# Kernel optimization log

Measured on AMD Instinct MI355X. Metric: run time of the kernel, lower is better.

Reference implementation:

```python
import jax, jax.numpy as jnp
import numpy as np

B, LQ, LK, D, H = 8, 1024, 1024, 1024, 8
DH = D // H  # per-head dim (att_units // num_heads, and V head dim since V = k)
LN_EPS = 1e-5


def setup_inputs() -> dict:
    key = jax.random.key(0)
    ks = jax.random.split(key, 8)
    s = 1.0 / np.sqrt(D)
    return {
        "q": jax.random.normal(ks[0], (B, LQ, D), dtype=jnp.float32),
        "k": jax.random.normal(ks[1], (B, LK, D), dtype=jnp.float32),
        "Wq": jax.random.normal(ks[2], (D, D), dtype=jnp.float32) * s,
        "bq": jnp.zeros((D,), dtype=jnp.float32),
        "Wk": jax.random.normal(ks[3], (D, D), dtype=jnp.float32) * s,
        "bk": jnp.zeros((D,), dtype=jnp.float32),
        "ln_gamma": jnp.ones((D,), dtype=jnp.float32),
        "ln_beta": jnp.zeros((D,), dtype=jnp.float32),
    }


def _layer_norm(x, gamma, beta):
    mu = jnp.mean(x, axis=-1, keepdims=True)
    var = jnp.mean(jnp.square(x - mu), axis=-1, keepdims=True)
    return (x - mu) * jax.lax.rsqrt(var + LN_EPS) * gamma + beta


def reference(q, k, Wq, bq, Wk, bk, ln_gamma, ln_beta):
    # q: [B, LQ, D], k: [B, LK, D]
    Q = q @ Wq + bq                      # [B, LQ, D]
    K = k @ Wk + bk                      # [B, LK, D]
    V = k                                # V is the raw key input (no projection)
    Qh = Q.reshape(B, LQ, H, DH)         # split(att_units//H, -1)+concat(0) == head reshape
    Kh = K.reshape(B, LK, H, DH)
    Vh = V.reshape(B, LK, H, DH)
    sim = jnp.einsum("bqhd,bkhd->bhqk", Qh, Kh) / np.sqrt(DH).astype(np.float32)
    attn = jax.nn.softmax(sim, axis=-1)  # [B, H, LQ, LK]
    att_h = jnp.einsum("bhqk,bkhd->bqhd", attn, Vh).reshape(B, LQ, D)
    att_h = att_h * 0.1 + q * 0.9        # residual blend
    att_h = _layer_norm(att_h, ln_gamma, ln_beta)
    return att_h  # ff_units_list == [] -> ff is None -> ff_h = att_h
```

## Files before the change

kernel.cpp:

```cpp
#include <hip/hip_runtime.h>
#include <hip/hip_bf16.h>
#include <cstdint>

#define BATCH 8
#define SEQ   1024
#define DMODEL 1024
#define NHEAD 8
#define DHEAD 128

using short8 = __attribute__((ext_vector_type(8))) short;
using f32x4  = __attribute__((ext_vector_type(4))) float;
typedef unsigned short u16;

__device__ inline u16 f2bf(float f) {
    union { float f; uint32_t u; } v; v.f = f;
    uint32_t r = (v.u + 0x7FFFu + ((v.u >> 16) & 1u)) >> 16;
    return (u16)r;
}

__device__ inline float exp2_fast(float x) { return __builtin_amdgcn_exp2f(x); }

__device__ inline uint32_t cvtpk_bf16(float a, float b) {
    uint32_t r;
    asm("v_cvt_pk_bf16_f32 %0, %1, %2" : "=v"(r) : "v"(a), "v"(b));
    return r;
}

#define GLL16(g, l)                                                                        \
    __builtin_amdgcn_global_load_lds((__attribute__((address_space(1))) const uint32_t*)(g), \
                                     (__attribute__((address_space(3))) uint32_t*)(l), 16, 0, 0)

__global__ __launch_bounds__(256) void conv_bf16(const float* __restrict__ q,
                                                 u16* __restrict__ dst) {
    size_t e = ((size_t)blockIdx.x * 256 + threadIdx.x) * 8;
    float4 a = *(const float4*)(q + e);
    float4 b = *(const float4*)(q + e + 4);
    uint4 r;
    r.x = (uint32_t)f2bf(a.x) | ((uint32_t)f2bf(a.y) << 16);
    r.y = (uint32_t)f2bf(a.z) | ((uint32_t)f2bf(a.w) << 16);
    r.z = (uint32_t)f2bf(b.x) | ((uint32_t)f2bf(b.y) << 16);
    r.w = (uint32_t)f2bf(b.z) | ((uint32_t)f2bf(b.w) << 16);
    *(uint4*)(dst + e) = r;
}

__global__ void transpose_conv(const float* __restrict__ Wq,
                               const float* __restrict__ Wk,
                               const float* __restrict__ kin,
                               u16* __restrict__ WqT,
                               u16* __restrict__ WkT,
                               u16* __restrict__ Vt,
                               u16* __restrict__ kb) {
    __shared__ float tile[32][33];
    int z = blockIdx.z;
    const float* src;
    u16* dst;
    u16* sdst = nullptr;
    if (z == 0)      { src = Wq; dst = WqT; }
    else if (z == 1) { src = Wk; dst = WkT; }
    else {
        src  = kin + (size_t)(z - 2) * DMODEL * SEQ;
        dst  = Vt  + (size_t)(z - 2) * DMODEL * SEQ;
        sdst = kb  + (size_t)(z - 2) * DMODEL * SEQ;
    }
    int x  = blockIdx.x * 32 + threadIdx.x;
    int y0 = blockIdx.y * 32;
    for (int i = threadIdx.y; i < 32; i += 8) {
        float v = src[(size_t)(y0 + i) * 1024 + x];
        tile[i][threadIdx.x] = v;
        if (sdst) sdst[(size_t)(y0 + i) * 1024 + x] = f2bf(v);
    }
    __syncthreads();
    int xo  = y0 + threadIdx.x;
    int yo0 = blockIdx.x * 32;
    for (int i = threadIdx.y; i < 32; i += 8)
        dst[(size_t)(yo0 + i) * 1024 + xo] = f2bf(tile[threadIdx.x][i]);
}

__global__ __launch_bounds__(256, 4) void gemm_dual(const u16* __restrict__ Aq,
                                                    const u16* __restrict__ Ak,
                                                    const u16* __restrict__ BTq,
                                                    const u16* __restrict__ BTk,
                                                    const float* __restrict__ biasq,
                                                    const float* __restrict__ biask,
                                                    u16* __restrict__ Outq,
                                                    u16* __restrict__ Outk) {
    __shared__ __align__(16) u16 As[2][128 * 32];
    __shared__ __align__(16) u16 Bs[2][128 * 32];

    int bid = blockIdx.x;
    int half = bid >> 9;
    int b2 = bid & 511;
    const u16* A  = half ? Ak  : Aq;
    const u16* BT = half ? BTk : BTq;
    const float* bias = half ? biask : biasq;
    u16* Out = half ? Outk : Outq;
    float scale = half ? 1.0f : (0.08838834764831845f * 1.4426950408889634f);

    int swz = (b2 & 7) * 64 + (b2 >> 3);
    int mt = swz >> 3, nt = swz & 7;
    int m0 = mt * 128, n0 = nt * 128;

    int t = threadIdx.x, lane = t & 63, w = t >> 6;
    int wm = w >> 1, wn = w & 1;
    int lr = lane & 15, lg = lane >> 4;

    const u16* pa[2];
    const u16* pb[2];
#pragma unroll
    for (int i = 0; i < 2; ++i) {
        int L = (w * 2 + i) * 64 + lane;
        int rp = L >> 3, ss = L & 7;
        int u = ss ^ (rp & 7);
        int row = (rp << 1) | (u >> 2);
        int g = u & 3;
        pa[i] = A  + (size_t)(m0 + row) * 1024 + g * 8;
        pb[i] = BT + (size_t)(n0 + row) * 1024 + g * 8;
    }
    int aoff[4], boff[4];
#pragma unroll
    for (int f = 0; f < 4; ++f) {
        int rowA = wm * 64 + f * 16 + lr;
        int sA = (((rowA & 1) << 2) | lg) ^ ((rowA >> 1) & 7);
        aoff[f] = (rowA >> 1) * 64 + sA * 8;
        int rowB = wn * 64 + f * 16 + lr;
        int sB = (((rowB & 1) << 2) | lg) ^ ((rowB >> 1) & 7);
        boff[f] = (rowB >> 1) * 64 + sB * 8;
    }

    f32x4 acc[4][4] = {};

#define GSTAGE(buf)                                         \
    {                                                       \
        _Pragma("unroll")                                   \
        for (int i = 0; i < 2; ++i) {                       \
            GLL16(pa[i], &As[buf][(w * 2 + i) * 512]);      \
            GLL16(pb[i], &Bs[buf][(w * 2 + i) * 512]);      \
            pa[i] += 32;                                    \
            pb[i] += 32;                                    \
        }                                                   \
    }

    GSTAGE(0);
    __syncthreads();

    int cur = 0;
    for (int k0 = 0; k0 < DMODEL; k0 += 32) {
        if (k0 + 32 < DMODEL) GSTAGE(cur ^ 1);
        short8 af[4], bfr[4];
#pragma unroll
        for (int f = 0; f < 4; ++f) {
            af[f]  = *(const short8*)&As[cur][aoff[f]];
            bfr[f] = *(const short8*)&Bs[cur][boff[f]];
        }
        __builtin_amdgcn_s_setprio(1);
#pragma unroll
        for (int fm = 0; fm < 4; ++fm)
#pragma unroll
            for (int fn = 0; fn < 4; ++fn)
                acc[fm][fn] = __builtin_amdgcn_mfma_f32_16x16x32_bf16(af[fm], bfr[fn], acc[fm][fn], 0, 0, 0);
        __builtin_amdgcn_s_setprio(0);
        __syncthreads();
        cur ^= 1;
    }
#undef GSTAGE

#pragma unroll
    for (int fn = 0; fn < 4; ++fn) {
        int col = n0 + wn * 64 + fn * 16 + lr;
        float bv = bias[col];
#pragma unroll
        for (int fm = 0; fm < 4; ++fm)
#pragma unroll
            for (int j = 0; j < 4; ++j) {
                int row = m0 + wm * 64 + fm * 16 + lg * 4 + j;
                Out[(size_t)row * 1024 + col] = f2bf((acc[fm][fn][j] + bv) * scale);
            }
    }
}

__global__ __launch_bounds__(512, 4) void attn_kernel(const u16* __restrict__ Qb,
                                                      const u16* __restrict__ Kb,
                                                      const u16* __restrict__ Vt,
                                                      float* __restrict__ AO) {
    __shared__ __align__(16) u16 Kbuf[2][64 * 128];
    __shared__ __align__(16) u16 Vbuf[2][128 * 64];
    __shared__ __align__(16) u16 Pl[8][16 * 64];

    int bid = blockIdx.x;
    int swz = (bid & 7) * 64 + (bid >> 3);
    int bh  = swz >> 3;
    int qt  = swz & 7;
    int b = bh >> 3, h = bh & 7;
    int q0 = qt * 128;

    int t = threadIdx.x, lane = t & 63, w = t >> 6;
    int lr = lane & 15, lg = lane >> 4;

    short8 qf[4];
    {
        size_t qbase = (size_t)(b * SEQ + q0 + w * 16 + lr) * 1024 + h * DHEAD;
#pragma unroll
        for (int kk = 0; kk < 4; ++kk)
            qf[kk] = *(const short8*)&Qb[qbase + kk * 32 + lg * 8];
    }

    float m_i = -1e30f, l_i = 0.f;
    f32x4 o[8] = {};
    u16* Pw = &Pl[w][0];
    const int pwrow = lr * 64;
    const int lx = lr & 7;

#define STAGE(nb, kk0)                                                                   \
    {                                                                                    \
        _Pragma("unroll")                                                                \
        for (int i = 0; i < 2; ++i) {                                                    \
            int g = (w * 2 + i) * 64 + lane;                                             \
            int row = g >> 4, cp = g & 15;                                               \
            int c = cp ^ (row & 7);                                                      \
            const u16* src = Kb + ((size_t)(b * SEQ + (kk0) + row) * 1024 + h * 128 + c * 8); \
            GLL16(src, &Kbuf[nb][(w * 2 + i) * 512]);                                    \
        }                                                                                \
        _Pragma("unroll")                                                                \
        for (int i = 0; i < 2; ++i) {                                                    \
            int g = (w * 2 + i) * 64 + lane;                                             \
            int d = g >> 3, cp = g & 7;                                                  \
            int c = cp ^ (d & 7);                                                        \
            const u16* src = Vt + ((size_t)(bh * 128 + d) * 1024 + (kk0) + c * 8);       \
            GLL16(src, &Vbuf[nb][(w * 2 + i) * 512]);                                    \
        }                                                                                \
    }

    STAGE(0, 0);
    __syncthreads();

    int cur = 0;
    for (int k0 = 0; k0 < SEQ; k0 += 64) {
        if (k0 + 64 < SEQ) STAGE(cur ^ 1, k0 + 64);

        const u16* Kc = &Kbuf[cur][0];
        f32x4 s[4] = {};
        __builtin_amdgcn_s_setprio(1);
#pragma unroll
        for (int fn = 0; fn < 4; ++fn) {
            int krow = (fn * 16 + lr) * 128;
#pragma unroll
            for (int kk = 0; kk < 4; ++kk) {
                short8 kf = *(const short8*)&Kc[krow + (((kk * 4 + lg) ^ lx) << 3)];
                s[fn] = __builtin_amdgcn_mfma_f32_16x16x32_bf16(kf, qf[kk], s[fn], 0, 0, 0);
            }
        }
        __builtin_amdgcn_s_setprio(0);

        float pmax = s[0][0];
#pragma unroll
        for (int fn = 0; fn < 4; ++fn)
#pragma unroll
            for (int j = 0; j < 4; ++j) pmax = fmaxf(pmax, s[fn][j]);
        pmax = fmaxf(pmax, __shfl_xor(pmax, 16));
        pmax = fmaxf(pmax, __shfl_xor(pmax, 32));

        if (__any(pmax > m_i + 11.5416f)) {
            float mnew = fmaxf(m_i, pmax);
            float alpha = exp2_fast(m_i - mnew);
            m_i = mnew;
            l_i *= alpha;
#pragma unroll
            for (int db = 0; db < 8; ++db) o[db] *= alpha;
        }

        float p[4][4];
        float lsum = 0.f;
#pragma unroll
        for (int fn = 0; fn < 4; ++fn)
#pragma unroll
            for (int j = 0; j < 4; ++j) {
                p[fn][j] = exp2_fast(s[fn][j] - m_i);
                lsum += p[fn][j];
            }
        lsum += __shfl_xor(lsum, 16);
        lsum += __shfl_xor(lsum, 32);
        l_i += lsum;

#pragma unroll
        for (int fn = 0; fn < 4; ++fn) {
            uint2 pk;
            pk.x = cvtpk_bf16(p[fn][0], p[fn][1]);
            pk.y = cvtpk_bf16(p[fn][2], p[fn][3]);
            int idx = pwrow + (((fn * 2 + (lg >> 1)) ^ lx) << 3) + ((lg & 1) << 2);
            *(uint2*)&Pw[idx] = pk;
        }

        const u16* Vc = &Vbuf[cur][0];
        short8 pf0 = *(const short8*)&Pw[pwrow + ((lg ^ lx) << 3)];
        short8 pf1 = *(const short8*)&Pw[pwrow + (((4 + lg) ^ lx) << 3)];
        __builtin_amdgcn_s_setprio(1);
#pragma unroll
        for (int db = 0; db < 8; ++db) {
            int vr = (db * 16 + lr) * 64;
            short8 v0 = *(const short8*)&Vc[vr + ((lg ^ lx) << 3)];
            short8 v1 = *(const short8*)&Vc[vr + (((4 + lg) ^ lx) << 3)];
            o[db] = __builtin_amdgcn_mfma_f32_16x16x32_bf16(v0, pf0, o[db], 0, 0, 0);
            o[db] = __builtin_amdgcn_mfma_f32_16x16x32_bf16(v1, pf1, o[db], 0, 0, 0);
        }
        __builtin_amdgcn_s_setprio(0);

        __syncthreads();
        cur ^= 1;
    }

    float inv = 1.f / l_i;
    size_t obase = (size_t)(b * SEQ + q0 + w * 16 + lr) * 1024 + h * DHEAD + lg * 4;
#pragma unroll
    for (int db = 0; db < 8; ++db) {
        float4 ov;
        ov.x = o[db][0] * inv;
        ov.y = o[db][1] * inv;
        ov.z = o[db][2] * inv;
        ov.w = o[db][3] * inv;
        *(float4*)&AO[obase + db * 16] = ov;
    }
#undef STAGE
}

__global__ __launch_bounds__(256) void ln_kernel(float* __restrict__ AO,
                                                 const float* __restrict__ qin,
                                                 const float* __restrict__ gamma,
                                                 const float* __restrict__ beta,
                                                 float* __restrict__ out) {
    __shared__ float red[8];
    int row = blockIdx.x;
    int t = threadIdx.x;
    size_t base = (size_t)row * 1024 + t * 4;

    float4 a = *(const float4*)&AO[base];
    float4 qq = *(const float4*)&qin[base];
    float x0 = a.x * 0.1f + qq.x * 0.9f;
    float x1 = a.y * 0.1f + qq.y * 0.9f;
    float x2 = a.z * 0.1f + qq.z * 0.9f;
    float x3 = a.w * 0.1f + qq.w * 0.9f;

    float s  = x0 + x1 + x2 + x3;
    float s2 = x0 * x0 + x1 * x1 + x2 * x2 + x3 * x3;
    for (int d = 1; d < 64; d <<= 1) {
        s  += __shfl_xor(s, d);
        s2 += __shfl_xor(s2, d);
    }
    int w = t >> 6, lane = t & 63;
    if (lane == 0) { red[w] = s; red[4 + w] = s2; }
    __syncthreads();
    s  = red[0] + red[1] + red[2] + red[3];
    s2 = red[4] + red[5] + red[6] + red[7];

    float mu   = s * (1.f / 1024.f);
    float var  = s2 * (1.f / 1024.f) - mu * mu;
    float rstd = rsqrtf(var + 1e-5f);

    float4 g  = *(const float4*)&gamma[t * 4];
    float4 be = *(const float4*)&beta[t * 4];
    float4 o;
    o.x = (x0 - mu) * rstd * g.x + be.x;
    o.y = (x1 - mu) * rstd * g.y + be.y;
    o.z = (x2 - mu) * rstd * g.z + be.z;
    o.w = (x3 - mu) * rstd * g.w + be.w;
    *(float4*)&out[base] = o;
}

extern "C" void kernel_launch(void* const* d_in, const int* in_sizes, int n_in,
                              void* d_out, int out_size, void* d_ws, size_t ws_size,
                              hipStream_t stream) {
    const float* q     = (const float*)d_in[0];
    const float* k     = (const float*)d_in[1];
    const float* Wq    = (const float*)d_in[2];
    const float* bq    = (const float*)d_in[3];
    const float* Wk    = (const float*)d_in[4];
    const float* bk    = (const float*)d_in[5];
    const float* gamma = (const float*)d_in[6];
    const float* beta  = (const float*)d_in[7];
    float* out = (float*)d_out;

    char* ws = (char*)d_ws;
    u16* WqT = (u16*)ws;
    u16* WkT = (u16*)(ws + (size_t)(2  << 20));
    u16* Qb  = (u16*)(ws + (size_t)(4  << 20));
    u16* Kb  = (u16*)(ws + (size_t)(20 << 20));
    u16* Vt  = (u16*)(ws + (size_t)(36 << 20));

    u16* qb = (u16*)d_out;
    u16* kb = qb + (size_t)8 * 1024 * 1024;

    conv_bf16<<<4096, 256, 0, stream>>>(q, qb);

    transpose_conv<<<dim3(32, 32, 2 + BATCH), dim3(32, 8), 0, stream>>>(Wq, Wk, k, WqT, WkT, Vt, kb);

    gemm_dual<<<1024, 256, 0, stream>>>(qb, kb, WqT, WkT, bq, bk, Qb, Kb);

    attn_kernel<<<512, 512, 0, stream>>>(Qb, Kb, Vt, out);

    ln_kernel<<<8192, 256, 0, stream>>>(out, q, gamma, beta, out);
}
```

Measured before the change: 135.1 us.

## Fuse fp32-to-bf16 activation conversion into projection GEMM and defer softmax row-sum reduction

Removes the separate conv_bf16 kernel and the bf16 copy of k written by transpose_conv. The projection GEMM now loads fp32 q/k directly into registers, converts them to bf16 and stores them into LDS after the MFMA block, while the B operand keeps its async global-to-LDS load. In attention, the cross-lane shuffles for the row max run only when a rescale is needed, and the row-sum shuffles are deferred to the end using per-lane partial sums. The GEMM doubles its A-side global reads in fp32 and uses more registers, in exchange for fewer kernel launches and less intermediate traffic.

Result: faster. 130.7 us (-3.2%).

```diff
diff --git a/kernel.cpp b/kernel.cpp
--- a/kernel.cpp
+++ b/kernel.cpp
@@ -30,45 +30,26 @@
     __builtin_amdgcn_global_load_lds((__attribute__((address_space(1))) const uint32_t*)(g), \
                                      (__attribute__((address_space(3))) uint32_t*)(l), 16, 0, 0)
 
-__global__ __launch_bounds__(256) void conv_bf16(const float* __restrict__ q,
-                                                 u16* __restrict__ dst) {
-    size_t e = ((size_t)blockIdx.x * 256 + threadIdx.x) * 8;
-    float4 a = *(const float4*)(q + e);
-    float4 b = *(const float4*)(q + e + 4);
-    uint4 r;
-    r.x = (uint32_t)f2bf(a.x) | ((uint32_t)f2bf(a.y) << 16);
-    r.y = (uint32_t)f2bf(a.z) | ((uint32_t)f2bf(a.w) << 16);
-    r.z = (uint32_t)f2bf(b.x) | ((uint32_t)f2bf(b.y) << 16);
-    r.w = (uint32_t)f2bf(b.z) | ((uint32_t)f2bf(b.w) << 16);
-    *(uint4*)(dst + e) = r;
-}
-
 __global__ void transpose_conv(const float* __restrict__ Wq,
                                const float* __restrict__ Wk,
                                const float* __restrict__ kin,
                                u16* __restrict__ WqT,
                                u16* __restrict__ WkT,
-                               u16* __restrict__ Vt,
-                               u16* __restrict__ kb) {
+                               u16* __restrict__ Vt) {
     __shared__ float tile[32][33];
     int z = blockIdx.z;
     const float* src;
     u16* dst;
-    u16* sdst = nullptr;
     if (z == 0)      { src = Wq; dst = WqT; }
     else if (z == 1) { src = Wk; dst = WkT; }
     else {
-        src  = kin + (size_t)(z - 2) * DMODEL * SEQ;
-        dst  = Vt  + (size_t)(z - 2) * DMODEL * SEQ;
-        sdst = kb  + (size_t)(z - 2) * DMODEL * SEQ;
+        src = kin + (size_t)(z - 2) * DMODEL * SEQ;
+        dst = Vt  + (size_t)(z - 2) * DMODEL * SEQ;
     }
     int x  = blockIdx.x * 32 + threadIdx.x;
     int y0 = blockIdx.y * 32;
-    for (int i = threadIdx.y; i < 32; i += 8) {
-        float v = src[(size_t)(y0 + i) * 1024 + x];
-        tile[i][threadIdx.x] = v;
-        if (sdst) sdst[(size_t)(y0 + i) * 1024 + x] = f2bf(v);
-    }
+    for (int i = threadIdx.y; i < 32; i += 8)
+        tile[i][threadIdx.x] = src[(size_t)(y0 + i) * 1024 + x];
     __syncthreads();
     int xo  = y0 + threadIdx.x;
     int yo0 = blockIdx.x * 32;
@@ -76,8 +57,8 @@
         dst[(size_t)(yo0 + i) * 1024 + xo] = f2bf(tile[threadIdx.x][i]);
 }
 
-__global__ __launch_bounds__(256, 4) void gemm_dual(const u16* __restrict__ Aq,
-                                                    const u16* __restrict__ Ak,
+__global__ __launch_bounds__(256, 4) void gemm_dual(const float* __restrict__ Aqf,
+                                                    const float* __restrict__ Akf,
                                                     const u16* __restrict__ BTq,
                                                     const u16* __restrict__ BTk,
                                                     const float* __restrict__ biasq,
@@ -90,8 +71,8 @@
     int bid = blockIdx.x;
     int half = bid >> 9;
     int b2 = bid & 511;
-    const u16* A  = half ? Ak  : Aq;
-    const u16* BT = half ? BTk : BTq;
+    const float* A  = half ? Akf : Aqf;
+    const u16* BT   = half ? BTk : BTq;
     const float* bias = half ? biask : biasq;
     u16* Out = half ? Outk : Outq;
     float scale = half ? 1.0f : (0.08838834764831845f * 1.4426950408889634f);
@@ -104,8 +85,9 @@
     int wm = w >> 1, wn = w & 1;
     int lr = lane & 15, lg = lane >> 4;
 
-    const u16* pa[2];
+    const float* pa[2];
     const u16* pb[2];
+    int ldsoff[2];
 #pragma unroll
     for (int i = 0; i < 2; ++i) {
         int L = (w * 2 + i) * 64 + lane;
@@ -115,6 +97,7 @@
         int g = u & 3;
         pa[i] = A  + (size_t)(m0 + row) * 1024 + g * 8;
         pb[i] = BT + (size_t)(n0 + row) * 1024 + g * 8;
+        ldsoff[i] = L * 8;
     }
     int aoff[4], boff[4];
 #pragma unroll
@@ -129,23 +112,36 @@
 
     f32x4 acc[4][4] = {};
 
-#define GSTAGE(buf)                                         \
-    {                                                       \
-        _Pragma("unroll")                                   \
-        for (int i = 0; i < 2; ++i) {                       \
-            GLL16(pa[i], &As[buf][(w * 2 + i) * 512]);      \
-            GLL16(pb[i], &Bs[buf][(w * 2 + i) * 512]);      \
-            pa[i] += 32;                                    \
-            pb[i] += 32;                                    \
-        }                                                   \
-    }
-
-    GSTAGE(0);
+#pragma unroll
+    for (int i = 0; i < 2; ++i) {
+        float4 v0 = *(const float4*)pa[i];
+        float4 v1 = *(const float4*)(pa[i] + 4);
+        uint4 r;
+        r.x = cvtpk_bf16(v0.x, v0.y);
+        r.y = cvtpk_bf16(v0.z, v0.w);
+        r.z = cvtpk_bf16(v1.x, v1.y);
+        r.w = cvtpk_bf16(v1.z, v1.w);
+        *(uint4*)&As[0][ldsoff[i]] = r;
+        GLL16(pb[i], &Bs[0][(w * 2 + i) * 512]);
+        pa[i] += 32;
+        pb[i] += 32;
+    }
     __syncthreads();
 
     int cur = 0;
     for (int k0 = 0; k0 < DMODEL; k0 += 32) {
-        if (k0 + 32 < DMODEL) GSTAGE(cur ^ 1);
+        bool more = (k0 + 32 < DMODEL);
+        float4 va[2], vb[2];
+        if (more) {
+#pragma unroll
+            for (int i = 0; i < 2; ++i) {
+                GLL16(pb[i], &Bs[cur ^ 1][(w * 2 + i) * 512]);
+                va[i] = *(const float4*)pa[i];
+                vb[i] = *(const float4*)(pa[i] + 4);
+                pa[i] += 32;
+                pb[i] += 32;
+            }
+        }
         short8 af[4], bfr[4];
 #pragma unroll
         for (int f = 0; f < 4; ++f) {
@@ -159,10 +155,20 @@
             for (int fn = 0; fn < 4; ++fn)
                 acc[fm][fn] = __builtin_amdgcn_mfma_f32_16x16x32_bf16(af[fm], bfr[fn], acc[fm][fn], 0, 0, 0);
         __builtin_amdgcn_s_setprio(0);
+        if (more) {
+#pragma unroll
+            for (int i = 0; i < 2; ++i) {
+                uint4 r;
+                r.x = cvtpk_bf16(va[i].x, va[i].y);
+                r.y = cvtpk_bf16(va[i].z, va[i].w);
+                r.z = cvtpk_bf16(vb[i].x, vb[i].y);
+                r.w = cvtpk_bf16(vb[i].z, vb[i].w);
+                *(uint4*)&As[cur ^ 1][ldsoff[i]] = r;
+            }
+        }
         __syncthreads();
         cur ^= 1;
     }
-#undef GSTAGE
 
 #pragma unroll
     for (int fn = 0; fn < 4; ++fn) {
@@ -204,7 +210,7 @@
             qf[kk] = *(const short8*)&Qb[qbase + kk * 32 + lg * 8];
     }
 
-    float m_i = -1e30f, l_i = 0.f;
+    float m_i = -1e30f, l_loc = 0.f;
     f32x4 o[8] = {};
     u16* Pw = &Pl[w][0];
     const int pwrow = lr * 64;
@@ -251,35 +257,34 @@
         }
         __builtin_amdgcn_s_setprio(0);
 
-        float pmax = s[0][0];
-#pragma unroll
-        for (int fn = 0; fn < 4; ++fn)
-#pragma unroll
-            for (int j = 0; j < 4; ++j) pmax = fmaxf(pmax, s[fn][j]);
-        pmax = fmaxf(pmax, __shfl_xor(pmax, 16));
-        pmax = fmaxf(pmax, __shfl_xor(pmax, 32));
+        float pm0 = fmaxf(fmaxf(s[0][0], s[0][1]), fmaxf(s[0][2], s[0][3]));
+        float pm1 = fmaxf(fmaxf(s[1][0], s[1][1]), fmaxf(s[1][2], s[1][3]));
+        float pm2 = fmaxf(fmaxf(s[2][0], s[2][1]), fmaxf(s[2][2], s[2][3]));
+        float pm3 = fmaxf(fmaxf(s[3][0], s[3][1]), fmaxf(s[3][2], s[3][3]));
+        float pmax = fmaxf(fmaxf(pm0, pm1), fmaxf(pm2, pm3));
 
         if (__any(pmax > m_i + 11.5416f)) {
-            float mnew = fmaxf(m_i, pmax);
+            float rm = pmax;
+            rm = fmaxf(rm, __shfl_xor(rm, 16));
+            rm = fmaxf(rm, __shfl_xor(rm, 32));
+            float mnew = fmaxf(m_i, rm);
             float alpha = exp2_fast(m_i - mnew);
             m_i = mnew;
-            l_i *= alpha;
+            l_loc *= alpha;
 #pragma unroll
             for (int db = 0; db < 8; ++db) o[db] *= alpha;
         }
 
         float p[4][4];
-        float lsum = 0.f;
-#pragma unroll
-        for (int fn = 0; fn < 4; ++fn)
-#pragma unroll
-            for (int j = 0; j < 4; ++j) {
-                p[fn][j] = exp2_fast(s[fn][j] - m_i);
-                lsum += p[fn][j];
-            }
-        lsum += __shfl_xor(lsum, 16);
-        lsum += __shfl_xor(lsum, 32);
-        l_i += lsum;
+        float ls0 = 0.f, ls1 = 0.f, ls2 = 0.f, ls3 = 0.f;
+#pragma unroll
+        for (int j = 0; j < 4; ++j) {
+            p[0][j] = exp2_fast(s[0][j] - m_i); ls0 += p[0][j];
+            p[1][j] = exp2_fast(s[1][j] - m_i); ls1 += p[1][j];
+            p[2][j] = exp2_fast(s[2][j] - m_i); ls2 += p[2][j];
+            p[3][j] = exp2_fast(s[3][j] - m_i); ls3 += p[3][j];
+        }
+        l_loc += (ls0 + ls1) + (ls2 + ls3);
 
 #pragma unroll
         for (int fn = 0; fn < 4; ++fn) {
@@ -308,7 +313,10 @@
         cur ^= 1;
     }
 
-    float inv = 1.f / l_i;
+    float lt = l_loc;
+    lt += __shfl_xor(lt, 16);
+    lt += __shfl_xor(lt, 32);
+    float inv = 1.f / lt;
     size_t obase = (size_t)(b * SEQ + q0 + w * 16 + lr) * 1024 + h * DHEAD + lg * 4;
 #pragma unroll
     for (int db = 0; db < 8; ++db) {
@@ -385,14 +393,9 @@
     u16* Kb  = (u16*)(ws + (size_t)(20 << 20));
     u16* Vt  = (u16*)(ws + (size_t)(36 << 20));
 
-    u16* qb = (u16*)d_out;
-    u16* kb = qb + (size_t)8 * 1024 * 1024;
-
-    conv_bf16<<<4096, 256, 0, stream>>>(q, qb);
-
-    transpose_conv<<<dim3(32, 32, 2 + BATCH), dim3(32, 8), 0, stream>>>(Wq, Wk, k, WqT, WkT, Vt, kb);
-
-    gemm_dual<<<1024, 256, 0, stream>>>(qb, kb, WqT, WkT, bq, bk, Qb, Kb);
+    transpose_conv<<<dim3(32, 32, 2 + BATCH), dim3(32, 8), 0, stream>>>(Wq, Wk, k, WqT, WkT, Vt);
+
+    gemm_dual<<<1024, 256, 0, stream>>>(q, k, WqT, WkT, bq, bk, Qb, Kb);
 
     attn_kernel<<<512, 512, 0, stream>>>(Qb, Kb, Vt, out);
 
```
